# Performance work log

Measured on AMD Instinct MI355X. Metric: run time of the kernel, lower is better.

Reference implementation:

```python
import jax, jax.numpy as jnp
import numpy as np

B, T, W, L, H = 32, 1024, 512, 12, 8
CH = W // H                      # per-head dim = 64
IN_CH = 3 + 6 + T                # x + params + class embedding channels = 1033
DFF = 4 * W
NEG = -100000.0
SCALE = 1.0 / np.sqrt(np.sqrt(CH))


def _layernorm(x, g, b, eps=1e-5):
    m = jnp.mean(x, axis=-1, keepdims=True)
    v = jnp.mean(jnp.square(x - m), axis=-1, keepdims=True)
    return (x - m) * jax.lax.rsqrt(v + eps) * g + b


def setup_inputs() -> dict:
    key = jax.random.key(0)
    ks = jax.random.split(key, 40)
    std = 0.25 * np.sqrt(1.0 / W)  # init_scale used inside Transformer

    def n(k, shape, s=std):
        return (jax.random.normal(k, shape, jnp.float32) * s).astype(jnp.float32)

    inp = {
        'x': jax.random.normal(ks[0], (B, 3, T), jnp.float32),
        'params': jax.random.normal(ks[1], (B, 6, T), jnp.float32),
        'mask': (jax.random.uniform(ks[2], (B, T)) > 0.2).astype(jnp.float32),
        'class_emb': jax.random.normal(ks[3], (T, T), jnp.float32),  # nn.Embedding(n_ctx, n_ctx)
        'w_in': n(ks[4], (IN_CH, W), 0.02), 'b_in': jnp.zeros((W,), jnp.float32),
        'ln_pre_g': jnp.ones((W,), jnp.float32), 'ln_pre_b': jnp.zeros((W,), jnp.float32),
        'qkv_w': n(ks[5], (L, W, 3 * W)), 'qkv_b': jnp.zeros((L, 3 * W), jnp.float32),
        'attn_pw': n(ks[6], (L, W, W)), 'attn_pb': jnp.zeros((L, W), jnp.float32),
        'ln1_g': jnp.ones((L, W), jnp.float32), 'ln1_b': jnp.zeros((L, W), jnp.float32),
        'fc_w': n(ks[7], (L, W, DFF)), 'fc_b': jnp.zeros((L, DFF), jnp.float32),
        'fcp_w': n(ks[8], (L, DFF, W)), 'fcp_b': jnp.zeros((L, W), jnp.float32),
        'ln2_g': jnp.ones((L, W), jnp.float32), 'ln2_b': jnp.zeros((L, W), jnp.float32),
        'ln_post_g': jnp.ones((W,), jnp.float32), 'ln_post_b': jnp.zeros((W,), jnp.float32),
        'w_out': n(ks[9], (W, W), 0.02), 'b_out': jnp.zeros((W,), jnp.float32),
        'agg_fc_w': n(ks[10], (W, DFF)), 'agg_fc_b': jnp.zeros((DFF,), jnp.float32),
        'agg_pw': n(ks[11], (DFF, W)), 'agg_pb': jnp.zeros((W,), jnp.float32),
    }
    return inp


def _block(h, p):
    qw, qb, pw, pb, l1g, l1b, fw, fb, gw, gb, l2g, l2b = p
    hn = _layernorm(h, l1g, l1b)
    qkv = (hn @ qw + qb).reshape(B, T, H, 3 * CH)
    q, k, v = jnp.split(qkv, 3, axis=-1)
    att = jnp.einsum('bthc,bshc->bhts', q * SCALE, k * SCALE)
    att = jax.nn.softmax(att.astype(jnp.float32), axis=-1)  # softmax in fp32
    o = jnp.einsum('bhts,bshc->bthc', att, v).reshape(B, T, W)
    h = h + o @ pw + pb
    hn2 = _layernorm(h, l2g, l2b)
    h = h + jax.nn.gelu(hn2 @ fw + fb, approximate=False) @ gw + gb
    return h, None


def reference(x, params, mask, class_emb, w_in, b_in, ln_pre_g, ln_pre_b,
              qkv_w, qkv_b, attn_pw, attn_pb, ln1_g, ln1_b, fc_w, fc_b,
              fcp_w, fcp_b, ln2_g, ln2_b, ln_post_g, ln_post_b, w_out, b_out,
              agg_fc_w, agg_fc_b, agg_pw, agg_pb):
    # concatenate params and class-embedding channels: [B, 1033, T]
    ce = jnp.broadcast_to(class_emb.T[None], (B, T, T))  # class_embed.transpose(1,2)
    xin = jnp.concatenate([x, params, ce], axis=1)
    h = jnp.einsum('bct,cw->btw', xin, w_in) + b_in      # input_proj on [B,T,1033]
    h = _layernorm(h, ln_pre_g, ln_pre_b)
    h, _ = jax.lax.scan(_block, h,
                        (qkv_w, qkv_b, attn_pw, attn_pb, ln1_g, ln1_b,
                         fc_w, fc_b, fcp_w, fcp_b, ln2_g, ln2_b))
    h = _layernorm(h, ln_post_g, ln_post_b)
    h = (h @ w_out + b_out).transpose(0, 2, 1)           # [B, 512, T]
    h = h * mask[:, None, :]
    pooled = jnp.max(h + (1.0 - mask[:, None, :]) * NEG, axis=2)  # [B, 512]
    z = jax.nn.gelu(pooled @ agg_fc_w + agg_fc_b, approximate=False) @ agg_pw + agg_pb
    return (z, h)
```

## Files before the change

### kernel.cpp

```cpp
#include <hip/hip_runtime.h>
#include <hip/hip_bf16.h>


typedef unsigned short u16;
typedef unsigned int u32;
typedef __attribute__((ext_vector_type(8))) short bf16x8;
typedef __attribute__((ext_vector_type(8))) unsigned short us8;
typedef __attribute__((ext_vector_type(4))) unsigned short us4;
typedef __attribute__((ext_vector_type(4))) float f32x4;

__device__ __forceinline__ float bf2f(u16 s) {
  union { u32 u; float f; } c; c.u = ((u32)s) << 16; return c.f;
}
__device__ __forceinline__ u16 f2bf(float f) {
  __hip_bfloat16 h = __float2bfloat16(f);
  union { __hip_bfloat16 h; u16 u; } c; c.h = h; return c.u;
}
__device__ __forceinline__ float gelu_f(float v) {
  return 0.5f * v * (1.0f + erff(v * 0.7071067811865475f));
}
__device__ __forceinline__ void gl2lds16(const u16* g, u16* l) {
  __builtin_amdgcn_global_load_lds((const __attribute__((address_space(1))) void*)g,
                                   (__attribute__((address_space(3))) void*)l, 16, 0, 0);
}
__device__ __forceinline__ f32x4 mfma16(bf16x8 a, bf16x8 b, f32x4 c) {
  return __builtin_amdgcn_mfma_f32_16x16x32_bf16(a, b, c, 0, 0, 0);
}
__device__ __forceinline__ int swz(int row) { return (row ^ (row >> 3)) & 7; }

template <int EPI>
__global__ __launch_bounds__(512)
void gemm_bt(const u16* __restrict__ A, const u16* __restrict__ Bt,
             const float* __restrict__ bias, float* __restrict__ Cf,
             u16* __restrict__ Cb, u16* __restrict__ Vt, int K, int lda, int ldb, int ldc)
{
  __shared__ __align__(16) u16 As[2][256 * 32];
  __shared__ __align__(16) u16 Bs[2][128 * 32];
  const int tid = threadIdx.x;
  const int lane = tid & 63, wid = tid >> 6;
  const int wm = wid & 3, wn = wid >> 2;
  const int nbx = gridDim.x;
  const int nwg = nbx * gridDim.y;
  int lin = blockIdx.y * nbx + blockIdx.x;
  lin = (lin & 7) * (nwg >> 3) + (lin >> 3);
  const long m0 = (long)(lin / nbx) * 256, n0 = (long)(lin % nbx) * 128;

  const int c0 = tid, c1 = tid + 512;
  const int kc0 = (c0 & 3) ^ (((c0 >> 2) >> 1) & 3);
  const int kc1 = (c1 & 3) ^ (((c1 >> 2) >> 1) & 3);
  const int kcb = (tid & 3) ^ (((tid >> 2) >> 1) & 3);
  const u16* aS0 = A + (m0 + (c0 >> 2)) * (long)lda + kc0 * 8;
  const u16* aS1 = A + (m0 + (c1 >> 2)) * (long)lda + kc1 * 8;
  const u16* bS0 = Bt + (n0 + (tid >> 2)) * (long)ldb + kcb * 8;

  f32x4 acc[4][4] = {};
  const int cl4 = lane & 15;
  const int gph = ((lane >> 4) ^ ((cl4 >> 1) & 3)) * 8;
  const int aro = (wm * 64 + cl4) * 32 + gph;
  const int bro = (wn * 64 + cl4) * 32 + gph;
  const int nt = K >> 5;

#define STAGE_AB(buf, k0_)                          \
  gl2lds16(aS0 + (k0_), As[buf] + c0 * 8);          \
  gl2lds16(aS1 + (k0_), As[buf] + c1 * 8);          \
  gl2lds16(bS0 + (k0_), Bs[buf] + tid * 8);

  STAGE_AB(0, 0);
  for (int t = 0; t < nt; ++t) {
    const int cur = t & 1;
    if (t < nt - 1) {
      STAGE_AB(cur ^ 1, (t + 1) * 32);
      asm volatile("s_waitcnt vmcnt(3)" ::: "memory");
    } else {
      asm volatile("s_waitcnt vmcnt(0)" ::: "memory");
    }
    __builtin_amdgcn_s_barrier();
    bf16x8 af[4], bfr[4];
#pragma unroll
    for (int i = 0; i < 4; ++i) af[i] = *(const bf16x8*)(As[cur] + aro + i * 16 * 32);
#pragma unroll
    for (int j = 0; j < 4; ++j) bfr[j] = *(const bf16x8*)(Bs[cur] + bro + j * 16 * 32);
    __builtin_amdgcn_s_setprio(1);
#pragma unroll
    for (int i = 0; i < 4; ++i)
#pragma unroll
      for (int j = 0; j < 4; ++j)
        acc[i][j] = mfma16(af[i], bfr[j], acc[i][j]);
    __builtin_amdgcn_s_setprio(0);
    __builtin_amdgcn_s_barrier();
  }
#undef STAGE_AB
  const int rg = (lane >> 4) * 4, cl = lane & 15;
#pragma unroll
  for (int i = 0; i < 4; ++i) {
#pragma unroll
    for (int j = 0; j < 4; ++j) {
      const long row = m0 + wm * 64 + i * 16 + rg;
      const long col = n0 + wn * 64 + j * 16 + cl;
      const float bv = bias ? bias[col] : 0.0f;
      if (EPI == 4) {
        const int hh = (int)col / 192, off = (int)col - hh * 192;
        if (off < 128) {
#pragma unroll
          for (int r = 0; r < 4; ++r)
            Cb[(row + r) * ldc + col] = f2bf(acc[i][j][r] + bv);
        } else {
          us4 pk;
#pragma unroll
          for (int r = 0; r < 4; ++r) pk[r] = f2bf(acc[i][j][r] + bv);
          const long bl = row >> 10, t0 = row & 1023;
          *(us4*)(Vt + (((bl * 8 + hh) * 64 + (off - 128)) << 10) + t0) = pk;
        }
      } else {
#pragma unroll
        for (int r = 0; r < 4; ++r) {
          float v = acc[i][j][r] + bv;
          long idx = (row + r) * ldc + col;
          if (EPI == 0) Cf[idx] = v;
          else if (EPI == 1) Cb[idx] = f2bf(v);
          else if (EPI == 2) Cf[idx] += v;
          else Cb[idx] = f2bf(gelu_f(v));
        }
      }
    }
  }
}

template <int EPI>
__global__ __launch_bounds__(1024)
void gemm_bt2(const u16* __restrict__ A, const u16* __restrict__ Bt,
              const float* __restrict__ bias, float* __restrict__ Cf,
              u16* __restrict__ Cb, int K, int lda, int ldb, int ldc)
{
  __shared__ __align__(16) u16 As[2][256 * 32];
  __shared__ __align__(16) u16 Bs[2][256 * 32];
  const int tid = threadIdx.x;
  const int lane = tid & 63, wid = tid >> 6;
  const int wm = wid & 3, wn = wid >> 2;
  const int nbx = gridDim.x;
  const int nwg = nbx * gridDim.y;
  int lin = blockIdx.y * nbx + blockIdx.x;
  lin = (lin & 7) * (nwg >> 3) + (lin >> 3);
  const long m0 = (long)(lin / nbx) * 256, n0 = (long)(lin % nbx) * 256;

  const int kcA = (tid & 3) ^ (((tid >> 2) >> 1) & 3);
  const u16* aS0 = A + (m0 + (tid >> 2)) * (long)lda + kcA * 8;
  const u16* bS0 = Bt + (n0 + (tid >> 2)) * (long)ldb + kcA * 8;

  f32x4 acc[4][4] = {};
  const int cl4 = lane & 15;
  const int gph = ((lane >> 4) ^ ((cl4 >> 1) & 3)) * 8;
  const int aro = (wm * 64 + cl4) * 32 + gph;
  const int bro = (wn * 64 + cl4) * 32 + gph;
  const int nt = K >> 5;

#define STAGE_AB2(buf, k0_)                         \
  gl2lds16(aS0 + (k0_), As[buf] + tid * 8);         \
  gl2lds16(bS0 + (k0_), Bs[buf] + tid * 8);

  STAGE_AB2(0, 0);
  for (int t = 0; t < nt; ++t) {
    const int cur = t & 1;
    if (t < nt - 1) {
      STAGE_AB2(cur ^ 1, (t + 1) * 32);
      asm volatile("s_waitcnt vmcnt(2)" ::: "memory");
    } else {
      asm volatile("s_waitcnt vmcnt(0)" ::: "memory");
    }
    __builtin_amdgcn_s_barrier();
    bf16x8 af[4], bfr[4];
#pragma unroll
    for (int i = 0; i < 4; ++i) af[i] = *(const bf16x8*)(As[cur] + aro + i * 16 * 32);
#pragma unroll
    for (int j = 0; j < 4; ++j) bfr[j] = *(const bf16x8*)(Bs[cur] + bro + j * 16 * 32);
    __builtin_amdgcn_s_setprio(1);
#pragma unroll
    for (int i = 0; i < 4; ++i)
#pragma unroll
      for (int j = 0; j < 4; ++j)
        acc[i][j] = mfma16(af[i], bfr[j], acc[i][j]);
    __builtin_amdgcn_s_setprio(0);
    __builtin_amdgcn_s_barrier();
  }
#undef STAGE_AB2
  const int rg = (lane >> 4) * 4, cl = lane & 15;
#pragma unroll
  for (int i = 0; i < 4; ++i) {
#pragma unroll
    for (int j = 0; j < 4; ++j) {
      const long row = m0 + wm * 64 + i * 16 + rg;
      const long col = n0 + wn * 64 + j * 16 + cl;
      const float bv = bias ? bias[col] : 0.0f;
#pragma unroll
      for (int r = 0; r < 4; ++r) {
        float v = acc[i][j][r] + bv;
        long idx = (row + r) * ldc + col;
        if (EPI == 0) Cf[idx] = v;
        else if (EPI == 1) Cb[idx] = f2bf(v);
        else if (EPI == 2) Cf[idx] += v;
        else Cb[idx] = f2bf(gelu_f(v));
      }
    }
  }
}

__global__ __launch_bounds__(512)
void attn_k(const u16* __restrict__ qkv, const u16* __restrict__ vt, u16* __restrict__ o)
{
  __shared__ __align__(16) u16 Qs[128 * 64];
  __shared__ __align__(16) u16 Ks[2][64 * 64];
  __shared__ __align__(16) u16 Vts[2][64 * 64];
  const int tid = threadIdx.x, lane = tid & 63, wid = tid >> 6;
  int lin = blockIdx.x;
  lin = (lin & 7) * 128 + (lin >> 3);
  const int qt = lin & 7, hh = (lin >> 3) & 7, b = lin >> 6;
  const long rowbase = (long)b * 1024;
  const long vbase = (((long)b * 8 + hh) * 64) * 1024;
  const int g = lane >> 4, cl = lane & 15;
  u16* Psw = Qs + wid * 1024;

#pragma unroll
  for (int it = 0; it < 2; ++it) {
    int c = tid + it * 512;
    int row = c >> 3, c8s = (c & 7) ^ swz(row);
    gl2lds16(qkv + (rowbase + qt * 128 + row) * 1536 + hh * 192 + c8s * 8, Qs + c * 8);
  }
#define STAGE_KV(buf, kt_)                                                            \
  {                                                                                   \
    int row = tid >> 3, c8s = (tid & 7) ^ swz(row);                                   \
    gl2lds16(qkv + (rowbase + (kt_) * 64 + row) * 1536 + hh * 192 + 64 + c8s * 8,     \
             Ks[buf] + tid * 8);                                                      \
    gl2lds16(vt + vbase + (long)row * 1024 + (kt_) * 64 + c8s * 8, Vts[buf] + tid * 8); \
  }
  STAGE_KV(0, 0);

  float m = -3.0e38f, l = 0.f;
  f32x4 oacc[4] = {};
  const int Rq = wid * 16 + cl, sq = swz(Rq) << 3;
  const int spw = swz(cl) << 3;
  bf16x8 aq[2];

  for (int kt = 0; kt < 16; ++kt) {
    const int cur = kt & 1;
    if (kt < 15) {
      STAGE_KV(cur ^ 1, kt + 1);
      asm volatile("s_waitcnt vmcnt(2)" ::: "memory");
    } else {
      asm volatile("s_waitcnt vmcnt(0)" ::: "memory");
    }
    __builtin_amdgcn_s_barrier();
    if (kt == 0) {
#pragma unroll
      for (int kb = 0; kb < 2; ++kb)
        aq[kb] = *(const bf16x8*)(Qs + Rq * 64 + ((kb * 32 + g * 8) ^ sq));
    }
    f32x4 s[4] = {};
    __builtin_amdgcn_s_setprio(1);
#pragma unroll
    for (int j = 0; j < 4; ++j) {
      const int Rk = j * 16 + cl, sk = swz(Rk) << 3;
#pragma unroll
      for (int kb = 0; kb < 2; ++kb) {
        bf16x8 bk = *(const bf16x8*)(Ks[cur] + Rk * 64 + ((kb * 32 + g * 8) ^ sk));
        s[j] = mfma16(bk, aq[kb], s[j]);
      }
    }
    __builtin_amdgcn_s_setprio(0);
    float mx = s[0][0];
#pragma unroll
    for (int j = 0; j < 4; ++j)
#pragma unroll
      for (int r = 0; r < 4; ++r) mx = fmaxf(mx, s[j][r]);
    mx *= 0.125f;
    mx = fmaxf(mx, __shfl_xor(mx, 16, 64));
    mx = fmaxf(mx, __shfl_xor(mx, 32, 64));
    if (!__all(mx <= m + 8.f)) {
      const float mnew = fmaxf(m, mx);
      const float al = __expf(m - mnew);
      m = mnew;
      l *= al;
      float alr[4];
#pragma unroll
      for (int r = 0; r < 4; ++r) alr[r] = __shfl(al, (lane & 48) | (g * 4 + r), 64);
#pragma unroll
      for (int cb = 0; cb < 4; ++cb) {
        f32x4 t = oacc[cb];
        t[0] *= alr[0]; t[1] *= alr[1]; t[2] *= alr[2]; t[3] *= alr[3];
        oacc[cb] = t;
      }
    }
    float p[4][4], ts = 0.f;
#pragma unroll
    for (int j = 0; j < 4; ++j)
#pragma unroll
      for (int r = 0; r < 4; ++r) {
        p[j][r] = __expf(s[j][r] * 0.125f - m);
        ts += p[j][r];
      }
    ts += __shfl_xor(ts, 16, 64);
    ts += __shfl_xor(ts, 32, 64);
    l += ts;
#pragma unroll
    for (int j = 0; j < 4; ++j) {
      us4 pk;
      pk[0] = f2bf(p[j][0]); pk[1] = f2bf(p[j][1]);
      pk[2] = f2bf(p[j][2]); pk[3] = f2bf(p[j][3]);
      *(us4*)(&Psw[cl * 64 + ((j * 16 + g * 4) ^ spw)]) = pk;
    }
    asm volatile("s_waitcnt lgkmcnt(0)" ::: "memory");
    bf16x8 pa[2];
#pragma unroll
    for (int kb = 0; kb < 2; ++kb)
      pa[kb] = *(const bf16x8*)(&Psw[cl * 64 + ((kb * 32 + g * 8) ^ spw)]);
    __builtin_amdgcn_s_setprio(1);
#pragma unroll
    for (int kb = 0; kb < 2; ++kb)
#pragma unroll
      for (int cb = 0; cb < 4; ++cb) {
        const int ch = cb * 16 + cl;
        bf16x8 vb = *(const bf16x8*)(Vts[cur] + ch * 64 + ((kb * 32 + g * 8) ^ (swz(ch) << 3)));
        oacc[cb] = mfma16(pa[kb], vb, oacc[cb]);
      }
    __builtin_amdgcn_s_setprio(0);
    __builtin_amdgcn_s_barrier();
  }
#undef STAGE_KV
  float lr[4];
#pragma unroll
  for (int r = 0; r < 4; ++r) lr[r] = __shfl(l, (lane & 48) | (g * 4 + r), 64);
#pragma unroll
  for (int cb = 0; cb < 4; ++cb)
#pragma unroll
    for (int r = 0; r < 4; ++r) {
      long row = rowbase + qt * 128 + wid * 16 + g * 4 + r;
      o[row * 512 + hh * 64 + cb * 16 + cl] = f2bf(oacc[cb][r] / lr[r]);
    }
}

template <int MODE>
__global__ __launch_bounds__(256)
void ln_k(const float* __restrict__ in_, const float* __restrict__ gg,
          const float* __restrict__ bb, void* __restrict__ out_)
{
  const long row = (long)blockIdx.x * 4 + (threadIdx.x >> 6);
  const int lane = threadIdx.x & 63;
  float x[8];
  const float* p = in_ + row * 512 + lane * 8;
  *(float4*)(x) = *(const float4*)(p);
  *(float4*)(x + 4) = *(const float4*)(p + 4);
  float s = 0.f;
#pragma unroll
  for (int j = 0; j < 8; ++j) s += x[j];
#pragma unroll
  for (int off = 1; off < 64; off <<= 1) s += __shfl_xor(s, off, 64);
  const float mean = s * (1.0f / 512.0f);
  float vs = 0.f;
#pragma unroll
  for (int j = 0; j < 8; ++j) { float d = x[j] - mean; vs += d * d; }
#pragma unroll
  for (int off = 1; off < 64; off <<= 1) vs += __shfl_xor(vs, off, 64);
  const float rstd = rsqrtf(vs * (1.0f / 512.0f) + 1e-5f);
  if (MODE == 0) {
    float y[8];
#pragma unroll
    for (int j = 0; j < 8; ++j)
      y[j] = (x[j] - mean) * rstd * gg[lane * 8 + j] + bb[lane * 8 + j];
    float* q = (float*)out_ + row * 512 + lane * 8;
    *(float4*)(q) = *(const float4*)(y);
    *(float4*)(q + 4) = *(const float4*)(y + 4);
  } else {
    us8 ov;
#pragma unroll
    for (int j = 0; j < 8; ++j)
      ov[j] = f2bf((x[j] - mean) * rstd * gg[lane * 8 + j] + bb[lane * 8 + j]);
    *(us8*)((u16*)out_ + row * 512 + lane * 8) = ov;
  }
}

__global__ __launch_bounds__(256)
void embed_k(const float* __restrict__ x, const float* __restrict__ par,
             const float* __restrict__ E, const float* __restrict__ w_in,
             const float* __restrict__ b_in, float* __restrict__ h)
{
  const long bt = blockIdx.x;
  const int b = (int)(bt >> 10), t = (int)(bt & 1023);
  float xs[9];
#pragma unroll
  for (int c = 0; c < 3; ++c) xs[c] = x[((long)b * 3 + c) * 1024 + t];
#pragma unroll
  for (int c = 0; c < 6; ++c) xs[3 + c] = par[((long)b * 6 + c) * 1024 + t];
  for (int w = threadIdx.x; w < 512; w += 256) {
    float a = E[(long)t * 512 + w] + b_in[w];
#pragma unroll
    for (int c = 0; c < 9; ++c) a += xs[c] * w_in[c * 512 + w];
    h[bt * 512 + w] = a;
  }
}

__global__ __launch_bounds__(256)
void tr_k(const float* __restrict__ in, u16* __restrict__ out, int R, int C)
{
  __shared__ u16 tile[32][33];
  const int r0 = blockIdx.y * 32, c0 = blockIdx.x * 32;
  const int tx = threadIdx.x & 31, ty = threadIdx.x >> 5;
  for (int rr = ty; rr < 32; rr += 8) tile[rr][tx] = f2bf(in[(long)(r0 + rr) * C + c0 + tx]);
  __syncthreads();
  for (int rr = ty; rr < 32; rr += 8) out[(long)(c0 + rr) * R + r0 + tx] = tile[tx][rr];
}

__global__ __launch_bounds__(256)
void trL_k(const float* __restrict__ qkv_w, const float* __restrict__ pw,
           const float* __restrict__ fcw, const float* __restrict__ fcpw,
           u16* __restrict__ o_qkv, u16* __restrict__ o_pw,
           u16* __restrict__ o_fc, u16* __restrict__ o_fcp)
{
  __shared__ u16 tile[32][33];
  int bid = blockIdx.x;
  const float* src; u16* dst; int R, C, bx, by;
  if (bid < 768)       { src = qkv_w; dst = o_qkv; R = 512;  C = 1536; bx = bid % 48; by = bid / 48; }
  else if (bid < 1024) { bid -= 768;  src = pw;   dst = o_pw;  R = 512;  C = 512;  bx = bid % 16; by = bid / 16; }
  else if (bid < 2048) { bid -= 1024; src = fcw;  dst = o_fc;  R = 512;  C = 2048; bx = bid % 64; by = bid / 64; }
  else                 { bid -= 2048; src = fcpw; dst = o_fcp; R = 2048; C = 512;  bx = bid % 16; by = bid / 16; }
  const int r0 = by * 32, c0 = bx * 32;
  const int tx = threadIdx.x & 31, ty = threadIdx.x >> 5;
  for (int rr = ty; rr < 32; rr += 8) tile[rr][tx] = f2bf(src[(long)(r0 + rr) * C + c0 + tx]);
  __syncthreads();
  for (int rr = ty; rr < 32; rr += 8) dst[(long)(c0 + rr) * R + r0 + tx] = tile[tx][rr];
}

__global__ __launch_bounds__(256)
void cast_k(const float* __restrict__ in, u16* __restrict__ out, long n)
{
  long i = ((long)blockIdx.x * 256 + threadIdx.x) * 4;
  if (i + 3 < n) {
    float4 v = *(const float4*)(in + i);
    out[i] = f2bf(v.x); out[i + 1] = f2bf(v.y); out[i + 2] = f2bf(v.z); out[i + 3] = f2bf(v.w);
  }
}

__global__ __launch_bounds__(256)
void pool1_k(const float* __restrict__ hm, const float* __restrict__ mask, float* __restrict__ part)
{
  const int c = blockIdx.x, b = blockIdx.y;
  const int t0 = c * 128;
  const int w0 = threadIdx.x, w1 = threadIdx.x + 256;
  float m0 = -3.0e38f, m1 = -3.0e38f;
  for (int t = 0; t < 128; ++t) {
    const float mv = mask[b * 1024 + t0 + t];
    const float neg = (1.0f - mv) * (-100000.0f);
    const float* row = hm + ((long)b * 1024 + t0 + t) * 512;
    m0 = fmaxf(m0, row[w0] * mv + neg);
    m1 = fmaxf(m1, row[w1] * mv + neg);
  }
  part[((long)b * 8 + c) * 512 + w0] = m0;
  part[((long)b * 8 + c) * 512 + w1] = m1;
}
__global__ __launch_bounds__(256)
void pool2_k(const float* __restrict__ part, float* __restrict__ pooled)
{
  const int b = blockIdx.y;
  const int w = blockIdx.x * 256 + threadIdx.x;
  float m = -3.0e38f;
#pragma unroll
  for (int c = 0; c < 8; ++c) m = fmaxf(m, part[((long)b * 8 + c) * 512 + w]);
  pooled[b * 512 + w] = m;
}

__global__ __launch_bounds__(256)
void tout_k(const float* __restrict__ hm, const float* __restrict__ mask, float* __restrict__ outh)
{
  __shared__ float tile[64][65];
  const int t0 = blockIdx.x * 64, w0 = blockIdx.y * 64, b = blockIdx.z;
  const int tx = threadIdx.x & 63, ty = threadIdx.x >> 6;
  for (int i = ty; i < 64; i += 4)
    tile[i][tx] = hm[((long)b * 1024 + t0 + i) * 512 + w0 + tx];
  __syncthreads();
  const float mv = mask[b * 1024 + t0 + tx];
  for (int i = ty; i < 64; i += 4)
    outh[((long)b * 512 + w0 + i) * 1024 + t0 + tx] = tile[tx][i] * mv;
}

__global__ __launch_bounds__(256)
void agg1p_k(const float* __restrict__ pooled, const float* __restrict__ wf,
             float* __restrict__ part)
{
  const int b = blockIdx.z, kc = blockIdx.y;
  const int n = blockIdx.x * 256 + threadIdx.x;
  float acc = 0.f;
  const int k0 = kc * 64;
#pragma unroll 8
  for (int k = 0; k < 64; ++k) acc += pooled[b * 512 + k0 + k] * wf[(long)(k0 + k) * 2048 + n];
  part[((long)b * 8 + kc) * 2048 + n] = acc;
}
__global__ __launch_bounds__(256)
void agg1c_k(const float* __restrict__ part, const float* __restrict__ bf_,
             float* __restrict__ z1)
{
  const int b = blockIdx.y;
  const int n = blockIdx.x * 256 + threadIdx.x;
  float acc = 0.f;
#pragma unroll
  for (int c = 0; c < 8; ++c) acc += part[((long)b * 8 + c) * 2048 + n];
  z1[(long)b * 2048 + n] = gelu_f(acc + bf_[n]);
}
__global__ __launch_bounds__(256)
void agg2p_k(const float* __restrict__ z1, const float* __restrict__ wp,
             float* __restrict__ part)
{
  const int b = blockIdx.z, kc = blockIdx.y;
  const int n = blockIdx.x * 256 + threadIdx.x;
  float acc = 0.f;
  const int k0 = kc * 256;
#pragma unroll 8
  for (int k = 0; k < 256; ++k) acc += z1[(long)b * 2048 + k0 + k] * wp[(long)(k0 + k) * 512 + n];
  part[((long)b * 8 + kc) * 512 + n] = acc;
}
__global__ __launch_bounds__(256)
void agg2c_k(const float* __restrict__ part, const float* __restrict__ bp,
             float* __restrict__ zo)
{
  const int b = blockIdx.y;
  const int n = blockIdx.x * 256 + threadIdx.x;
  float acc = 0.f;
#pragma unroll
  for (int c = 0; c < 8; ++c) acc += part[((long)b * 8 + c) * 512 + n];
  zo[b * 512 + n] = acc + bp[n];
}

extern "C" void kernel_launch(void* const* d_in, const int* in_sizes, int n_in,
                              void* d_out, int out_size, void* d_ws, size_t ws_size,
                              hipStream_t stream)
{
  (void)in_sizes; (void)n_in; (void)out_size; (void)ws_size;
  const float* x        = (const float*)d_in[0];
  const float* params   = (const float*)d_in[1];
  const float* mask     = (const float*)d_in[2];
  const float* class_emb= (const float*)d_in[3];
  const float* w_in     = (const float*)d_in[4];
  const float* b_in     = (const float*)d_in[5];
  const float* ln_pre_g = (const float*)d_in[6];
  const float* ln_pre_b = (const float*)d_in[7];
  const float* qkv_w    = (const float*)d_in[8];
  const float* qkv_b    = (const float*)d_in[9];
  const float* attn_pw  = (const float*)d_in[10];
  const float* attn_pb  = (const float*)d_in[11];
  const float* ln1_g    = (const float*)d_in[12];
  const float* ln1_b    = (const float*)d_in[13];
  const float* fc_w     = (const float*)d_in[14];
  const float* fc_b     = (const float*)d_in[15];
  const float* fcp_w    = (const float*)d_in[16];
  const float* fcp_b    = (const float*)d_in[17];
  const float* ln2_g    = (const float*)d_in[18];
  const float* ln2_b    = (const float*)d_in[19];
  const float* ln_post_g= (const float*)d_in[20];
  const float* ln_post_b= (const float*)d_in[21];
  const float* w_out    = (const float*)d_in[22];
  const float* b_out    = (const float*)d_in[23];
  const float* agg_fc_w = (const float*)d_in[24];
  const float* agg_fc_b = (const float*)d_in[25];
  const float* agg_pw   = (const float*)d_in[26];
  const float* agg_pb   = (const float*)d_in[27];

  float* out_f = (float*)d_out;
  float* out_h = out_f + 16384;
  u16* sc = (u16*)out_h;

  char* ws = (char*)d_ws;
  float* hf = (float*)ws;       ws += (size_t)32768 * 512 * 4;
  u16* hn = (u16*)ws;           ws += (size_t)32768 * 512 * 2;
  float* E = (float*)ws;        ws += (size_t)1024 * 512 * 4;
  u16* ce_b = (u16*)ws;         ws += (size_t)1024 * 1024 * 2;
  u16* wt_qkv = (u16*)ws;       ws += (size_t)1536 * 512 * 2;
  u16* wt_pw  = (u16*)ws;       ws += (size_t)512 * 512 * 2;
  u16* wt_fc  = (u16*)ws;       ws += (size_t)2048 * 512 * 2;
  u16* wt_fcp = (u16*)ws;       ws += (size_t)512 * 2048 * 2;
  u16* w_in_t = (u16*)ws;       ws += (size_t)512 * 1024 * 2;
  u16* w_out_t= (u16*)ws;       ws += (size_t)512 * 512 * 2;
  float* pooled = (float*)ws;   ws += (size_t)32 * 512 * 4;
  float* z1     = (float*)ws;   ws += (size_t)32 * 2048 * 4;
  float* part   = (float*)ws;   ws += (size_t)32 * 8 * 512 * 4;
  float* apart1 = (float*)ws;   ws += (size_t)32 * 8 * 2048 * 4;
  float* apart2 = (float*)ws;   ws += (size_t)32 * 8 * 512 * 4;
  u16* vt       = (u16*)ws;     ws += (size_t)16 * 8 * 64 * 1024 * 2;

  cast_k<<<1024, 256, 0, stream>>>(class_emb, ce_b, 1024 * 1024);
  tr_k<<<dim3(16, 32), 256, 0, stream>>>(w_in + 9 * 512, w_in_t, 1024, 512);
  tr_k<<<dim3(16, 16), 256, 0, stream>>>(w_out, w_out_t, 512, 512);
  gemm_bt<0><<<dim3(4, 4), 512, 0, stream>>>(ce_b, w_in_t, nullptr, E, nullptr, nullptr,
                                             1024, 1024, 1024, 512);
  embed_k<<<32768, 256, 0, stream>>>(x, params, E, w_in, b_in, hf);
  ln_k<0><<<8192, 256, 0, stream>>>(hf, ln_pre_g, ln_pre_b, hf);

  for (int l = 0; l < 12; ++l) {
    trL_k<<<3072, 256, 0, stream>>>(qkv_w + (size_t)l * 512 * 1536,
                                    attn_pw + (size_t)l * 512 * 512,
                                    fc_w + (size_t)l * 512 * 2048,
                                    fcp_w + (size_t)l * 2048 * 512,
                                    wt_qkv, wt_pw, wt_fc, wt_fcp);

    ln_k<1><<<8192, 256, 0, stream>>>(hf, ln1_g + l * 512, ln1_b + l * 512, hn);
    for (int half = 0; half < 2; ++half) {
      const size_t ro = (size_t)half * 16384;
      gemm_bt<4><<<dim3(12, 64), 512, 0, stream>>>(hn + ro * 512, wt_qkv, qkv_b + l * 1536,
                                                   nullptr, sc, vt, 512, 512, 512, 1536);
      attn_k<<<1024, 512, 0, stream>>>(sc, vt, hn + ro * 512);
    }
    gemm_bt<2><<<dim3(4, 128), 512, 0, stream>>>(hn, wt_pw, attn_pb + l * 512,
                                                 hf, nullptr, nullptr, 512, 512, 512, 512);
    ln_k<1><<<8192, 256, 0, stream>>>(hf, ln2_g + l * 512, ln2_b + l * 512, hn);
    for (int half = 0; half < 2; ++half) {
      const size_t ro = (size_t)half * 16384;
      gemm_bt2<3><<<dim3(8, 64), 1024, 0, stream>>>(hn + ro * 512, wt_fc, fc_b + l * 2048,
                                                    nullptr, sc, 512, 512, 512, 2048);
      gemm_bt<2><<<dim3(4, 64), 512, 0, stream>>>(sc, wt_fcp, fcp_b + l * 512,
                                                  hf + ro * 512, nullptr, nullptr, 2048, 2048, 2048, 512);
    }
  }

  ln_k<1><<<8192, 256, 0, stream>>>(hf, ln_post_g, ln_post_b, hn);
  gemm_bt<0><<<dim3(4, 128), 512, 0, stream>>>(hn, w_out_t, b_out, hf, nullptr, nullptr,
                                               512, 512, 512, 512);
  pool1_k<<<dim3(8, 32), 256, 0, stream>>>(hf, mask, part);
  pool2_k<<<dim3(2, 32), 256, 0, stream>>>(part, pooled);
  agg1p_k<<<dim3(8, 8, 32), 256, 0, stream>>>(pooled, agg_fc_w, apart1);
  agg1c_k<<<dim3(8, 32), 256, 0, stream>>>(apart1, agg_fc_b, z1);
  agg2p_k<<<dim3(2, 8, 32), 256, 0, stream>>>(z1, agg_pw, apart2);
  agg2c_k<<<dim3(2, 32), 256, 0, stream>>>(apart2, agg_pb, out_f);
  tout_k<<<dim3(16, 8, 32), 256, 0, stream>>>(hf, mask, out_h);
}
```

Before: 6.518 ms.

## Add 128x128 GEMM for FC projection and shrink attention LDS footprint

After: 6.436 ms. No clear change (-1.3%).

```diff
diff --git a/kernel.cpp b/kernel.cpp
--- a/kernel.cpp
+++ b/kernel.cpp
@@ -127,6 +127,90 @@
 }
 
 template <int EPI>
+__global__ __launch_bounds__(256)
+void gemm_bt1(const u16* __restrict__ A, const u16* __restrict__ Bt,
+              const float* __restrict__ bias, float* __restrict__ Cf,
+              u16* __restrict__ Cb, int K, int lda, int ldb, int ldc)
+{
+  __shared__ __align__(16) u16 As[2][128 * 32];
+  __shared__ __align__(16) u16 Bs[2][128 * 32];
+  const int tid = threadIdx.x;
+  const int lane = tid & 63, wid = tid >> 6;
+  const int wm = wid >> 1, wn = wid & 1;
+  const int nbx = gridDim.x;
+  const int nwg = nbx * gridDim.y;
+  int lin = blockIdx.y * nbx + blockIdx.x;
+  lin = (lin & 7) * (nwg >> 3) + (lin >> 3);
+  const long m0 = (long)(lin / nbx) * 128, n0 = (long)(lin % nbx) * 128;
+
+  const int c0 = tid, c1 = tid + 256;
+  const int kc0 = (c0 & 3) ^ (((c0 >> 2) >> 1) & 3);
+  const int kc1 = (c1 & 3) ^ (((c1 >> 2) >> 1) & 3);
+  const u16* aS0 = A + (m0 + (c0 >> 2)) * (long)lda + kc0 * 8;
+  const u16* aS1 = A + (m0 + (c1 >> 2)) * (long)lda + kc1 * 8;
+  const u16* bS0 = Bt + (n0 + (c0 >> 2)) * (long)ldb + kc0 * 8;
+  const u16* bS1 = Bt + (n0 + (c1 >> 2)) * (long)ldb + kc1 * 8;
+
+  f32x4 acc[4][4] = {};
+  const int cl4 = lane & 15;
+  const int gph = ((lane >> 4) ^ ((cl4 >> 1) & 3)) * 8;
+  const int aro = (wm * 64 + cl4) * 32 + gph;
+  const int bro = (wn * 64 + cl4) * 32 + gph;
+  const int nt = K >> 5;
+
+#define STAGE_AB1(buf, k0_)                         \
+  gl2lds16(aS0 + (k0_), As[buf] + c0 * 8);          \
+  gl2lds16(aS1 + (k0_), As[buf] + c1 * 8);          \
+  gl2lds16(bS0 + (k0_), Bs[buf] + c0 * 8);          \
+  gl2lds16(bS1 + (k0_), Bs[buf] + c1 * 8);
+
+  STAGE_AB1(0, 0);
+  for (int t = 0; t < nt; ++t) {
+    const int cur = t & 1;
+    if (t < nt - 1) {
+      STAGE_AB1(cur ^ 1, (t + 1) * 32);
+      asm volatile("s_waitcnt vmcnt(4)" ::: "memory");
+    } else {
+      asm volatile("s_waitcnt vmcnt(0)" ::: "memory");
+    }
+    __builtin_amdgcn_s_barrier();
+    bf16x8 af[4], bfr[4];
+#pragma unroll
+    for (int i = 0; i < 4; ++i) af[i] = *(const bf16x8*)(As[cur] + aro + i * 16 * 32);
+#pragma unroll
+    for (int j = 0; j < 4; ++j) bfr[j] = *(const bf16x8*)(Bs[cur] + bro + j * 16 * 32);
+    __builtin_amdgcn_s_setprio(1);
+#pragma unroll
+    for (int i = 0; i < 4; ++i)
+#pragma unroll
+      for (int j = 0; j < 4; ++j)
+        acc[i][j] = mfma16(af[i], bfr[j], acc[i][j]);
+    __builtin_amdgcn_s_setprio(0);
+    __builtin_amdgcn_s_barrier();
+  }
+#undef STAGE_AB1
+  const int rg = (lane >> 4) * 4, cl = lane & 15;
+#pragma unroll
+  for (int i = 0; i < 4; ++i) {
+#pragma unroll
+    for (int j = 0; j < 4; ++j) {
+      const long row = m0 + wm * 64 + i * 16 + rg;
+      const long col = n0 + wn * 64 + j * 16 + cl;
+      const float bv = bias ? bias[col] : 0.0f;
+#pragma unroll
+      for (int r = 0; r < 4; ++r) {
+        float v = acc[i][j][r] + bv;
+        long idx = (row + r) * ldc + col;
+        if (EPI == 0) Cf[idx] = v;
+        else if (EPI == 1) Cb[idx] = f2bf(v);
+        else if (EPI == 2) Cf[idx] += v;
+        else Cb[idx] = f2bf(gelu_f(v));
+      }
+    }
+  }
+}
+
+template <int EPI>
 __global__ __launch_bounds__(1024)
 void gemm_bt2(const u16* __restrict__ A, const u16* __restrict__ Bt,
               const float* __restrict__ bias, float* __restrict__ Cf,
@@ -207,9 +291,9 @@
 __global__ __launch_bounds__(512)
 void attn_k(const u16* __restrict__ qkv, const u16* __restrict__ vt, u16* __restrict__ o)
 {
-  __shared__ __align__(16) u16 Qs[128 * 64];
   __shared__ __align__(16) u16 Ks[2][64 * 64];
   __shared__ __align__(16) u16 Vts[2][64 * 64];
+  __shared__ __align__(16) u16 Ps[8][512];
   const int tid = threadIdx.x, lane = tid & 63, wid = tid >> 6;
   int lin = blockIdx.x;
   lin = (lin & 7) * 128 + (lin >> 3);
@@ -217,13 +301,15 @@
   const long rowbase = (long)b * 1024;
   const long vbase = (((long)b * 8 + hh) * 64) * 1024;
   const int g = lane >> 4, cl = lane & 15;
-  u16* Psw = Qs + wid * 1024;
-
-#pragma unroll
-  for (int it = 0; it < 2; ++it) {
-    int c = tid + it * 512;
-    int row = c >> 3, c8s = (c & 7) ^ swz(row);
-    gl2lds16(qkv + (rowbase + qt * 128 + row) * 1536 + hh * 192 + c8s * 8, Qs + c * 8);
+  u16* Psw = Ps[wid];
+  const int Rq = wid * 16 + cl;
+  const int sw2 = ((cl >> 1) & 3) << 3;
+
+  bf16x8 aq[2];
+  {
+    const u16* qp = qkv + (rowbase + qt * 128 + Rq) * 1536 + hh * 192 + g * 8;
+    aq[0] = *(const bf16x8*)(qp);
+    aq[1] = *(const bf16x8*)(qp + 32);
   }
 #define STAGE_KV(buf, kt_)                                                            \
   {                                                                                   \
@@ -236,9 +322,6 @@
 
   float m = -3.0e38f, l = 0.f;
   f32x4 oacc[4] = {};
-  const int Rq = wid * 16 + cl, sq = swz(Rq) << 3;
-  const int spw = swz(cl) << 3;
-  bf16x8 aq[2];
 
   for (int kt = 0; kt < 16; ++kt) {
     const int cur = kt & 1;
@@ -249,11 +332,6 @@
       asm volatile("s_waitcnt vmcnt(0)" ::: "memory");
     }
     __builtin_amdgcn_s_barrier();
-    if (kt == 0) {
-#pragma unroll
-      for (int kb = 0; kb < 2; ++kb)
-        aq[kb] = *(const bf16x8*)(Qs + Rq * 64 + ((kb * 32 + g * 8) ^ sq));
-    }
     f32x4 s[4] = {};
     __builtin_amdgcn_s_setprio(1);
 #pragma unroll
@@ -301,27 +379,25 @@
     ts += __shfl_xor(ts, 32, 64);
     l += ts;
 #pragma unroll
-    for (int j = 0; j < 4; ++j) {
-      us4 pk;
-      pk[0] = f2bf(p[j][0]); pk[1] = f2bf(p[j][1]);
-      pk[2] = f2bf(p[j][2]); pk[3] = f2bf(p[j][3]);
-      *(us4*)(&Psw[cl * 64 + ((j * 16 + g * 4) ^ spw)]) = pk;
-    }
-    asm volatile("s_waitcnt lgkmcnt(0)" ::: "memory");
-    bf16x8 pa[2];
-#pragma unroll
-    for (int kb = 0; kb < 2; ++kb)
-      pa[kb] = *(const bf16x8*)(&Psw[cl * 64 + ((kb * 32 + g * 8) ^ spw)]);
-    __builtin_amdgcn_s_setprio(1);
-#pragma unroll
-    for (int kb = 0; kb < 2; ++kb)
+    for (int kb = 0; kb < 2; ++kb) {
+#pragma unroll
+      for (int jj = 0; jj < 2; ++jj) {
+        us4 pk;
+        pk[0] = f2bf(p[2 * kb + jj][0]); pk[1] = f2bf(p[2 * kb + jj][1]);
+        pk[2] = f2bf(p[2 * kb + jj][2]); pk[3] = f2bf(p[2 * kb + jj][3]);
+        *(us4*)(&Psw[cl * 32 + ((jj * 16 + g * 4) ^ sw2)]) = pk;
+      }
+      asm volatile("s_waitcnt lgkmcnt(0)" ::: "memory");
+      bf16x8 pa = *(const bf16x8*)(&Psw[cl * 32 + ((g * 8) ^ sw2)]);
+      __builtin_amdgcn_s_setprio(1);
 #pragma unroll
       for (int cb = 0; cb < 4; ++cb) {
         const int ch = cb * 16 + cl;
         bf16x8 vb = *(const bf16x8*)(Vts[cur] + ch * 64 + ((kb * 32 + g * 8) ^ (swz(ch) << 3)));
-        oacc[cb] = mfma16(pa[kb], vb, oacc[cb]);
+        oacc[cb] = mfma16(pa, vb, oacc[cb]);
       }
-    __builtin_amdgcn_s_setprio(0);
+      __builtin_amdgcn_s_setprio(0);
+    }
     __builtin_amdgcn_s_barrier();
   }
 #undef STAGE_KV
@@ -612,8 +688,8 @@
       const size_t ro = (size_t)half * 16384;
       gemm_bt2<3><<<dim3(8, 64), 1024, 0, stream>>>(hn + ro * 512, wt_fc, fc_b + l * 2048,
                                                     nullptr, sc, 512, 512, 512, 2048);
-      gemm_bt<2><<<dim3(4, 64), 512, 0, stream>>>(sc, wt_fcp, fcp_b + l * 512,
-                                                  hf + ro * 512, nullptr, nullptr, 2048, 2048, 2048, 512);
+      gemm_bt1<2><<<dim3(4, 128), 256, 0, stream>>>(sc, wt_fcp, fcp_b + l * 512,
+                                                    hf + ro * 512, nullptr, 2048, 2048, 2048, 512);
     }
   }
 
```
